# Optimization experiments

Measured on AMD Instinct MI355X. Metric: run time of the kernel, lower is better.

## Reference

```python
import jax, jax.numpy as jnp
import numpy as np

KS = 5  # kernel_size


def _extract_patches(x, ks):
    # x: [B, C, H, W] -> [B, C, Ho, Wo, ks*ks] (VALID windows)
    B, C, H, W = x.shape
    Ho, Wo = H - ks + 1, W - ks + 1
    taps = [x[:, :, u:u + Ho, v:v + Wo] for u in range(ks) for v in range(ks)]
    return jnp.stack(taps, axis=-1)


def setup_inputs() -> dict:
    key = jax.random.key(0)
    k1, k2, k3 = jax.random.split(key, 3)
    B, C, H, W = 8, 3, 128, 128
    O, ks = 8, KS
    stdv = 1.0 / np.sqrt(C * ks * ks)
    x = jax.random.normal(k1, (B, C, H, W), dtype=jnp.float32)
    K_hit = jax.random.uniform(k2, (O, C, ks, ks), dtype=jnp.float32,
                               minval=-stdv, maxval=stdv)
    K_miss = jax.random.uniform(k3, (O, C, ks, ks), dtype=jnp.float32,
                                minval=-stdv, maxval=stdv)
    return {"x": x, "K_hit": K_hit, "K_miss": K_miss}


def reference(x, K_hit, K_miss):
    # Fmap[b, k*C+c, y, x] = min_{u,v}(patch - K_hit[k,c]) - max_{u,v}(patch - K_miss[k,c])
    O, C, ks, _ = K_hit.shape
    patches = _extract_patches(x, ks)                    # [B, C, Ho, Wo, ks*ks]
    B, _, Ho, Wo, P = patches.shape
    p = patches[:, None]                                 # [B, 1, C, Ho, Wo, P]
    kh = K_hit.reshape(O, C, P)[None, :, :, None, None, :]
    km = K_miss.reshape(O, C, P)[None, :, :, None, None, :]
    hit = jnp.min(p - kh, axis=-1)                       # [B, O, C, Ho, Wo]
    miss = jnp.max(p - km, axis=-1)                      # [B, O, C, Ho, Wo]
    fmap = hit - miss
    return fmap.reshape(B, O * C, Ho, Wo)
```

## Files before the change

kernel.cpp:

```cpp
#include <hip/hip_runtime.h>

#define B_   8
#define C_   3
#define O_   8
#define H_   128
#define W_   128
#define KS_  5
#define HO_  (H_ - KS_ + 1)
#define WO_  (W_ - KS_ + 1)
#define NPIX (HO_ * WO_)
#define NTAP (KS_ * KS_)
#define BLK  256

__global__ __launch_bounds__(BLK)
void mnn_kernel(const float* __restrict__ x,
                const float* __restrict__ Kh,
                const float* __restrict__ Km,
                float* __restrict__ out)
{
    __shared__ float sKh[O_ * NTAP];
    __shared__ float sKm[O_ * NTAP];

    const int bc = blockIdx.y;
    const int b  = bc / C_;
    const int c  = bc % C_;

    for (int i = threadIdx.x; i < O_ * NTAP; i += BLK) {
        const int o = i / NTAP;
        const int t = i % NTAP;
        const int g = o * (C_ * NTAP) + c * NTAP + t;
        sKh[i] = Kh[g];
        sKm[i] = Km[g];
    }
    __syncthreads();

    const int p = blockIdx.x * BLK + threadIdx.x;
    if (p >= NPIX) return;
    const int ho = p / WO_;
    const int wo = p % WO_;

    float patch[NTAP];
    const float* xrow = x + ((b * C_ + c) * H_ + ho) * W_ + wo;
#pragma unroll
    for (int u = 0; u < KS_; ++u)
#pragma unroll
        for (int v = 0; v < KS_; ++v)
            patch[u * KS_ + v] = xrow[u * W_ + v];

    const size_t obase = ((size_t)b * (O_ * C_) + c) * (size_t)NPIX + (size_t)ho * WO_ + wo;

#pragma unroll
    for (int o = 0; o < O_; ++o) {
        float hit  =  INFINITY;
        float miss = -INFINITY;
#pragma unroll
        for (int t = 0; t < NTAP; ++t) {
            hit  = fminf(hit,  patch[t] - sKh[o * NTAP + t]);
            miss = fmaxf(miss, patch[t] - sKm[o * NTAP + t]);
        }
        out[obase + (size_t)o * (C_ * NPIX)] = hit - miss;
    }
}

extern "C" void kernel_launch(void* const* d_in, const int* in_sizes, int n_in,
                              void* d_out, int out_size, void* d_ws, size_t ws_size,
                              hipStream_t stream)
{
    const float* x  = (const float*)d_in[0];
    const float* Kh = (const float*)d_in[1];
    const float* Km = (const float*)d_in[2];
    float* out = (float*)d_out;

    dim3 grid((NPIX + BLK - 1) / BLK, B_ * C_);
    dim3 block(BLK);
    mnn_kernel<<<grid, block, 0, stream>>>(x, Kh, Km, out);
}
```

Baseline: 66.64 us.

## Compute two output pixels per thread with float2 loads and direct weight reads

Each thread now computes two horizontally adjacent output pixels. It reuses a shared 5x6 input window held in registers, loads it with float2 vector reads, and writes results with float2 stores. The shared-memory staging of the kernel weights and the block barrier are removed, and weights are read directly from global memory. These uniform reads are likely scalarized or cached. The intent is to cut redundant input loads and per-pixel overhead, at the cost of half as many threads and more registers per thread.

```diff
diff --git a/kernel.cpp b/kernel.cpp
--- a/kernel.cpp
+++ b/kernel.cpp
@@ -1,16 +1,19 @@
 #include <hip/hip_runtime.h>
 
-#define B_   8
-#define C_   3
-#define O_   8
-#define H_   128
-#define W_   128
-#define KS_  5
-#define HO_  (H_ - KS_ + 1)
-#define WO_  (W_ - KS_ + 1)
-#define NPIX (HO_ * WO_)
-#define NTAP (KS_ * KS_)
-#define BLK  256
+#define B_    8
+#define C_    3
+#define O_    8
+#define H_    128
+#define W_    128
+#define KS_   5
+#define HO_   (H_ - KS_ + 1)
+#define WO_   (W_ - KS_ + 1)
+#define NPIX  (HO_ * WO_)
+#define NTAP  (KS_ * KS_)
+#define PX    2
+#define NG    (WO_ / PX)
+#define NPIXG (HO_ * NG)
+#define BLK   256
 
 __global__ __launch_bounds__(BLK)
 void mnn_kernel(const float* __restrict__ x,
@@ -18,47 +21,54 @@
                 const float* __restrict__ Km,
                 float* __restrict__ out)
 {
-    __shared__ float sKh[O_ * NTAP];
-    __shared__ float sKm[O_ * NTAP];
-
     const int bc = blockIdx.y;
     const int b  = bc / C_;
     const int c  = bc % C_;
 
-    for (int i = threadIdx.x; i < O_ * NTAP; i += BLK) {
-        const int o = i / NTAP;
-        const int t = i % NTAP;
-        const int g = o * (C_ * NTAP) + c * NTAP + t;
-        sKh[i] = Kh[g];
-        sKm[i] = Km[g];
+    const int p = blockIdx.x * BLK + threadIdx.x;
+    if (p >= NPIXG) return;
+    const int ho  = p / NG;
+    const int wo0 = (p % NG) * PX;
+
+    float w[KS_][KS_ + PX - 1];
+    const float* xrow = x + ((b * C_ + c) * H_ + ho) * W_ + wo0;
+#pragma unroll
+    for (int u = 0; u < KS_; ++u) {
+#pragma unroll
+        for (int v2 = 0; v2 < (KS_ + PX - 1 + 1) / 2; ++v2) {
+            const float2 t = *reinterpret_cast<const float2*>(xrow + u * W_ + v2 * 2);
+            w[u][v2 * 2 + 0] = t.x;
+            w[u][v2 * 2 + 1] = t.y;
+        }
     }
-    __syncthreads();
 
-    const int p = blockIdx.x * BLK + threadIdx.x;
-    if (p >= NPIX) return;
-    const int ho = p / WO_;
-    const int wo = p % WO_;
+    const float* khc = Kh + c * NTAP;
+    const float* kmc = Km + c * NTAP;
 
-    float patch[NTAP];
-    const float* xrow = x + ((b * C_ + c) * H_ + ho) * W_ + wo;
-#pragma unroll
-    for (int u = 0; u < KS_; ++u)
-#pragma unroll
-        for (int v = 0; v < KS_; ++v)
-            patch[u * KS_ + v] = xrow[u * W_ + v];
-
-    const size_t obase = ((size_t)b * (O_ * C_) + c) * (size_t)NPIX + (size_t)ho * WO_ + wo;
+    const size_t obase = ((size_t)b * (O_ * C_) + c) * (size_t)NPIX
+                       + (size_t)ho * WO_ + wo0;
 
 #pragma unroll
     for (int o = 0; o < O_; ++o) {
-        float hit  =  INFINITY;
-        float miss = -INFINITY;
+        float hit0  =  INFINITY, hit1  =  INFINITY;
+        float miss0 = -INFINITY, miss1 = -INFINITY;
 #pragma unroll
-        for (int t = 0; t < NTAP; ++t) {
-            hit  = fminf(hit,  patch[t] - sKh[o * NTAP + t]);
-            miss = fmaxf(miss, patch[t] - sKm[o * NTAP + t]);
+        for (int u = 0; u < KS_; ++u) {
+#pragma unroll
+            for (int v = 0; v < KS_; ++v) {
+                const int t = u * KS_ + v;
+                const float kh = khc[o * (C_ * NTAP) + t];
+                const float km = kmc[o * (C_ * NTAP) + t];
+                hit0  = fminf(hit0,  w[u][v]     - kh);
+                hit1  = fminf(hit1,  w[u][v + 1] - kh);
+                miss0 = fmaxf(miss0, w[u][v]     - km);
+                miss1 = fmaxf(miss1, w[u][v + 1] - km);
+            }
         }
-        out[obase + (size_t)o * (C_ * NPIX)] = hit - miss;
+        float2 r;
+        r.x = hit0 - miss0;
+        r.y = hit1 - miss1;
+        *reinterpret_cast<float2*>(out + obase + (size_t)o * (C_ * NPIX)) = r;
     }
 }
 
@@ -71,7 +81,7 @@
     const float* Km = (const float*)d_in[2];
     float* out = (float*)d_out;
 
-    dim3 grid((NPIX + BLK - 1) / BLK, B_ * C_);
+    dim3 grid((NPIXG + BLK - 1) / BLK, B_ * C_);
     dim3 block(BLK);
     mnn_kernel<<<grid, block, 0, stream>>>(x, Kh, Km, out);
 }
```

Measured after the change: 65.75 us. About the same (-1.3%).
